# Kernel tuning notes

Measured on AMD Instinct MI355X. Metric: run time of the kernel, lower is better.

The kernel has to match this reference:

```python
import jax, jax.numpy as jnp
import numpy as np

N, D = 8192, 512
HEADS, DIM_HEAD, M, ITERS = 8, 64, 256, 6
WP = 256          # CustomAttention weight_params_dim
E = 262144        # number of adjacency edges
K = 33            # residual depthwise conv kernel


def setup_inputs():
    key = jax.random.key(0)
    ks = jax.random.split(key, 12)
    inner = HEADS * DIM_HEAD
    xav = (6.0 / (D + WP)) ** 0.5
    return {
        "dense": jax.random.normal(ks[0], (N, D), jnp.float32),
        "adj_rows": jax.random.randint(ks[1], (E,), 0, N, dtype=jnp.int32),
        "adj_cols": jax.random.randint(ks[2], (E,), 0, N, dtype=jnp.int32),
        "adj_vals": jnp.ones((E,), jnp.float32),
        "wq": jax.random.uniform(ks[3], (D, WP), jnp.float32, -xav, xav),
        "wk": jax.random.uniform(ks[4], (D, WP), jnp.float32, -xav, xav),
        "w_qkv": jax.random.normal(ks[5], (3 * inner, D), jnp.float32) * D ** -0.5,
        "w_out": jax.random.normal(ks[6], (D, inner), jnp.float32) * inner ** -0.5,
        "b_out": jnp.zeros((D,), jnp.float32),
        "res_kernel": jax.random.normal(ks[7], (HEADS, 1, K, 1), jnp.float32) * 0.05,
        "wv_w": jax.random.normal(ks[8], (D, D), jnp.float32) * D ** -0.5,
        "wv_b": jnp.zeros((D,), jnp.float32),
    }


def _pinv(x, iters):
    # Moore-Penrose iterative pseudo-inverse (lucidrains nystrom-attention)
    ax = jnp.abs(x)
    z = jnp.swapaxes(x, -1, -2) / (ax.sum(-1).max() * ax.sum(-2).max())
    I = jnp.eye(x.shape[-1], dtype=x.dtype)
    for _ in range(iters):
        xz = x @ z
        z = 0.25 * z @ (13.0 * I - xz @ (15.0 * I - xz @ (7.0 * I - xz)))
    return z


def _nystrom(x, w_qkv, w_out, b_out, res_kernel):
    # x: [n, dim]; batch of 1 in original (squeezed here)
    n = x.shape[0]
    pad = (-n) % M
    xp = jnp.pad(x, ((pad, 0), (0, 0)))  # pad at front, as in original
    n_p = n + pad
    qkv = xp @ w_qkv.T  # [n_p, 3*h*d]
    q, k, v = [t.reshape(n_p, HEADS, DIM_HEAD).transpose(1, 0, 2)
               for t in jnp.split(qkv, 3, axis=-1)]  # each [h, n_p, d]
    q = q * DIM_HEAD ** -0.5
    l = n_p // M
    q_l = q.reshape(HEADS, M, l, DIM_HEAD).mean(2)  # [h, m, d] landmark means
    k_l = k.reshape(HEADS, M, l, DIM_HEAD).mean(2)
    a1 = jax.nn.softmax(jnp.einsum('hid,hjd->hij', q, k_l), -1)    # [h, n_p, m]
    a2 = jax.nn.softmax(jnp.einsum('hid,hjd->hij', q_l, k_l), -1)  # [h, m, m]
    a3 = jax.nn.softmax(jnp.einsum('hid,hjd->hij', q_l, k), -1)    # [h, m, n_p]
    out = (a1 @ _pinv(a2, ITERS)) @ (a3 @ v)  # [h, n_p, d]
    # residual depthwise conv over sequence dim, per head (groups=heads)
    res = jax.lax.conv_general_dilated(
        v[None], res_kernel, (1, 1), ((K // 2, K // 2), (0, 0)),
        dimension_numbers=('NCHW', 'OIHW', 'NCHW'), feature_group_count=HEADS)[0]
    out = out + res
    out = out.transpose(1, 0, 2).reshape(n_p, HEADS * DIM_HEAD) @ w_out.T + b_out
    return out[-n:]


def reference(dense, adj_rows, adj_cols, adj_vals, wq, wk, w_qkv, w_out, b_out,
              res_kernel, wv_w, wv_b):
    xg = _nystrom(dense, w_qkv, w_out, b_out, res_kernel)
    enc = xg + dense                              # [N, D]
    q = enc @ wq
    k = enc @ wk
    att = (q @ k.T) * (WP ** -0.5)                # [N, N] scaled logits
    # sparse adjacency mask + row-sum (torch.sparse.sum over dim=1)
    edge_scores = att[adj_rows, adj_cols] * adj_vals
    A_raw = jax.ops.segment_sum(edge_scores, adj_rows, num_segments=dense.shape[0])
    alpha = jax.nn.softmax(A_raw)                 # softmax over all N instances
    value = dense @ wv_w.T + wv_b                 # [N, D]
    xl = alpha[:, None] * value
    wei = jax.nn.sigmoid(-xl)
    sq = wei * wei
    xo = xl * 2.0 * sq + 2.0 * enc * (1.0 - sq)   # gated residual blend
    return xo, A_raw
```

## Files before the change

### kernel.cpp

```cpp
#include <hip/hip_runtime.h>
#include <hip/hip_bf16.h>

#define NSEQ 8192
#define DDIM 512
#define HEADS 8
#define DH 64
#define MLM 256
#define LSUB 32
#define WP 256
#define KCONV 33
#define INNER 512
#define QKV_LD 1536

static const size_t OFF_QKVBF  = 0;
static const size_t OFF_VT     = 6291456;
static const size_t OFF_SC     = 8388608;
static const size_t OFF_A2     = 8388608;
static const size_t OFF_Z0     = 8912896;
static const size_t OFF_Z1     = 9437184;
static const size_t OFF_P      = 9961472;
static const size_t OFF_T1     = 10485760;
static const size_t OFF_T2     = 11010048;
static const size_t OFF_QKE    = 10485760;
static const size_t OFF_ATTNBF = 12582912;
static const size_t OFF_ATTN   = 16777216;
static const size_t OFF_ENC    = 0;
static const size_t OFF_ENCBF  = 4194304;
static const size_t OFF_VAL    = 6291456;
static const size_t OFF_DENSEBF= 20971520;
static const size_t OFF_WQKVBF = 23068672;
static const size_t OFF_WOUTBF = 23461888;
static const size_t OFF_WQKT   = 23592960;
static const size_t OFF_WVBF   = 23724032;
static const size_t OFF_QL     = 23855104;
static const size_t OFF_KL     = 23986176;
static const size_t OFF_QLBF   = 24117248;
static const size_t OFF_KLSBF  = 24182784;
static const size_t OFF_A3V    = 24248320;
static const size_t OFF_BB     = 24379392;
static const size_t OFF_BBT    = 24510464;
static const size_t OFF_SCAL   = 24576000;
static const size_t OFF_ALPHA  = 24576016;
static const size_t OFF_DEN3   = 24584208;

__device__ __forceinline__ float bf2f(unsigned short u) {
    return __uint_as_float(((unsigned int)u) << 16);
}
__device__ __forceinline__ unsigned short f2bf(float x) {
    unsigned int u = __float_as_uint(x);
    u += 0x7FFFu + ((u >> 16) & 1u);
    return (unsigned short)(u >> 16);
}

typedef __attribute__((ext_vector_type(8))) short bf16x8;
typedef __attribute__((ext_vector_type(4))) float f32x4;

__device__ __forceinline__ void gload_lds16(const void* g, void* l) {
    __builtin_amdgcn_global_load_lds(
// ... 19 lines not shown
    const float* __restrict__ in, unsigned short* __restrict__ out, int R, int C)
{
    int idx = blockIdx.x * 256 + threadIdx.x;
    if (idx < R * C) {
        int oc = idx / R;
        int orow = idx % R;
        out[idx] = f2bf(in[(size_t)orow * C + oc]);
    }
}

__global__ __launch_bounds__(256) void gemm_mfma_ntb(
    const unsigned short* __restrict__ A, int lda, size_t sA,
    const unsigned short* __restrict__ B, int ldb, size_t sB,
    float* __restrict__ C, unsigned short* __restrict__ Cbf, int ldc, size_t sC,
    int K, const float* __restrict__ bias, const float* __restrict__ addsrc,
    int expmode)
{
    __shared__ __align__(16) unsigned short As[64 * 64];
    __shared__ __align__(16) unsigned short Bs[128 * 64];
    const int tid = threadIdx.x;
    const int wave = tid >> 6, lane = tid & 63;
    const int l15 = lane & 15, l4 = lane >> 4;
    const int wm = wave >> 1, wn = wave & 1;
    const size_t bm = (size_t)blockIdx.x * 64;
    const size_t bn = (size_t)blockIdx.y * 128;
    const int z = blockIdx.z;
    const unsigned short* Ab = A + (size_t)z * sA;
    const unsigned short* Bb = B + (size_t)z * sB;
    const int swzr = (l15 & 7) << 3;
    f32x4 acc[2][4] = {};
    for (int k0 = 0; k0 < K; k0 += 64) {
        __syncthreads();
#pragma unroll
        for (int c2 = 0; c2 < 2; ++c2) {
            int id = c2 * 256 + tid;
            int row = id >> 3;
            int cg = ((id & 7) ^ (row & 7)) << 3;
            gload_lds16(Ab + (bm + row) * (size_t)lda + k0 + cg, As + id * 8);
        }
#pragma unroll
        for (int c2 = 0; c2 < 4; ++c2) {
            int id = c2 * 256 + tid;
            int row = id >> 3;
            int cg = ((id & 7) ^ (row & 7)) << 3;
            gload_lds16(Bb + (bn + row) * (size_t)ldb + k0 + cg, Bs + id * 8);
        }
        __syncthreads();
#pragma unroll
        for (int c = 0; c < 2; ++c) {
            bf16x8 af[2], bfv[4];
#pragma unroll
            for (int i = 0; i < 2; ++i)
                af[i] = *reinterpret_cast<const bf16x8*>(
                    &As[(wm * 32 + i * 16 + l15) * 64 + ((c * 32 + l4 * 8) ^ swzr)]);
#pragma unroll
            for (int j = 0; j < 4; ++j)
                bfv[j] = *reinterpret_cast<const bf16x8*>(
                    &Bs[(wn * 64 + j * 16 + l15) * 64 + ((c * 32 + l4 * 8) ^ swzr)]);
#pragma unroll
            for (int i = 0; i < 2; ++i)
#pragma unroll
                for (int j = 0; j < 4; ++j)
                    acc[i][j] = __builtin_amdgcn_mfma_f32_16x16x32_bf16(
                        af[i], bfv[j], acc[i][j], 0, 0, 0);
        }
    }
    float* Cz = C ? C + (size_t)z * sC : nullptr;
    unsigned short* Cbz = Cbf ? Cbf + (size_t)z * sC : nullptr;
#pragma unroll
    for (int i = 0; i < 2; ++i)
#pragma unroll
        for (int j = 0; j < 4; ++j)
#pragma unroll
            for (int r = 0; r < 4; ++r) {
                size_t row = bm + wm * 32 + i * 16 + l4 * 4 + r;
                size_t col = bn + wn * 64 + j * 16 + l15;
                float v = acc[i][j][r];
                if (bias)   v += bias[col];
                if (addsrc) v += addsrc[row * (size_t)ldc + col];
                if (expmode) v = __expf(v);
                if (Cz)  Cz[row * (size_t)ldc + col] = v;
                if (Cbz) Cbz[row * (size_t)ldc + col] = f2bf(v);
            }
}

__global__ __launch_bounds__(256) void bmm_split(
    const float* __restrict__ A, const float* __restrict__ B, float* __restrict__ C,
    int K, int N, int ntn, size_t sA, size_t sB, size_t sC, float alpha, float beta)
{
    __shared__ __align__(16) unsigned short Ah[64 * 72], Al[64 * 72];
    __shared__ __align__(16) unsigned short Bh[64 * 72], Bl[64 * 72];
    const int tid = threadIdx.x;
    const int wave = tid >> 6, lane = tid & 63;
    const int l15 = lane & 15, l4 = lane >> 4;
    const int wm = wave >> 1, wn = wave & 1;
    const int b = blockIdx.y;
    const int tm = blockIdx.x / ntn, tn = blockIdx.x % ntn;
    const float* Ab = A + (size_t)b * sA;
    const float* Bb = B + (size_t)b * sB;
    float* Cb = C + (size_t)b * sC;
    const int arow = tid >> 2, akq = (tid & 3) * 16;
    const int kp = tid & 31, nc = tid >> 5;
    f32x4 acc[2][2] = {};
    for (int k0 = 0; k0 < K; k0 += 64) {
        __syncthreads();
#pragma unroll
        for (int s = 0; s < 4; ++s) {
            float4 a = *reinterpret_cast<const float4*>(Ab + (size_t)(tm * 64 + arow) * K + k0 + akq + s * 4);
            unsigned short h0 = f2bf(a.x), h1 = f2bf(a.y), h2 = f2bf(a.z), h3 = f2bf(a.w);
            unsigned short g0 = f2bf(a.x - bf2f(h0)), g1 = f2bf(a.y - bf2f(h1));
            unsigned short g2 = f2bf(a.z - bf2f(h2)), g3 = f2bf(a.w - bf2f(h3));
            uint2 ph, pl;
            ph.x = h0 | ((unsigned int)h1 << 16); ph.y = h2 | ((unsigned int)h3 << 16);
            pl.x = g0 | ((unsigned int)g1 << 16); pl.y = g2 | ((unsigned int)g3 << 16);
            *reinterpret_cast<uint2*>(&Ah[arow * 72 + akq + s * 4]) = ph;
            *reinterpret_cast<uint2*>(&Al[arow * 72 + akq + s * 4]) = pl;
        }
#pragma unroll
        for (int s = 0; s < 2; ++s) {
            int cb = nc * 8 + s * 4;
            float4 b0 = *reinterpret_cast<const float4*>(Bb + (size_t)(k0 + 2 * kp) * N + tn * 64 + cb);
            float4 b1 = *reinterpret_cast<const float4*>(Bb + (size_t)(k0 + 2 * kp + 1) * N + tn * 64 + cb);
            float x0[4] = {b0.x, b0.y, b0.z, b0.w};
            float x1[4] = {b1.x, b1.y, b1.z, b1.w};
#pragma unroll
            for (int c = 0; c < 4; ++c) {
                unsigned short h0 = f2bf(x0[c]), h1 = f2bf(x1[c]);
                unsigned short g0 = f2bf(x0[c] - bf2f(h0)), g1 = f2bf(x1[c] - bf2f(h1));
                *reinterpret_cast<unsigned int*>(&Bh[(cb + c) * 72 + 2 * kp]) =
                    h0 | ((unsigned int)h1 << 16);
                *reinterpret_cast<unsigned int*>(&Bl[(cb + c) * 72 + 2 * kp]) =
                    g0 | ((unsigned int)g1 << 16);
            }
        }
        __syncthreads();
#pragma unroll
        for (int ks = 0; ks < 2; ++ks) {
            bf16x8 ah[2], al[2], bh[2], bl[2];
#pragma unroll
            for (int i = 0; i < 2; ++i) {
                int rr = (wm * 32 + i * 16 + l15) * 72 + ks * 32 + l4 * 8;
                ah[i] = *reinterpret_cast<const bf16x8*>(&Ah[rr]);
                al[i] = *reinterpret_cast<const bf16x8*>(&Al[rr]);
            }
#pragma unroll
            for (int j = 0; j < 2; ++j) {
                int rr = (wn * 32 + j * 16 + l15) * 72 + ks * 32 + l4 * 8;
                bh[j] = *reinterpret_cast<const bf16x8*>(&Bh[rr]);
                bl[j] = *reinterpret_cast<const bf16x8*>(&Bl[rr]);
            }
#pragma unroll
            for (int i = 0; i < 2; ++i)
#pragma unroll
                for (int j = 0; j < 2; ++j) {
                    acc[i][j] = __builtin_amdgcn_mfma_f32_16x16x32_bf16(ah[i], bh[j], acc[i][j], 0, 0, 0);
                    acc[i][j] = __builtin_amdgcn_mfma_f32_16x16x32_bf16(ah[i], bl[j], acc[i][j], 0, 0, 0);
                    acc[i][j] = __builtin_amdgcn_mfma_f32_16x16x32_bf16(al[i], bh[j], acc[i][j], 0, 0, 0);
                }
        }
    }
#pragma unroll
    for (int i = 0; i < 2; ++i)
#pragma unroll
        for (int j = 0; j < 2; ++j)
#pragma unroll
            for (int r = 0; r < 4; ++r) {
                int row = tm * 64 + wm * 32 + i * 16 + l4 * 4 + r;
                int col = tn * 64 + wn * 32 + j * 16 + l15;
                float v = beta * acc[i][j][r];
                if (alpha != 0.f) v += alpha * Ab[(size_t)row * K + col];
                Cb[(size_t)row * N + col] = v;
            }
}

__global__ __launch_bounds__(256) void pv3_mfma(
    const unsigned short* __restrict__ sc, const unsigned short* __restrict__ vT,
    float* __restrict__ part)
{
    __shared__ __align__(16) unsigned short As[64 * 64];
    __shared__ __align__(16) unsigned short Bs[64 * 64];
    const int tid = threadIdx.x;
    const int wave = tid >> 6, lane = tid & 63;
    const int l15 = lane & 15, l4 = lane >> 4;
    const int wm = wave >> 1, wn = wave & 1;
    const int it = blockIdx.x, kc = blockIdx.y, h = blockIdx.z;
    const unsigned short* Ap = sc + (size_t)h * MLM * NSEQ + (size_t)(it * 64) * NSEQ + kc * 512;
// ... 37 lines not shown
    }
    float* Cp = part + ((size_t)(kc * 8 + h) * MLM + it * 64) * DH;
#pragma unroll
    for (int i = 0; i < 2; ++i)
#pragma unroll
        for (int j = 0; j < 2; ++j)
#pragma unroll
            for (int r = 0; r < 4; ++r)
                Cp[(wm * 32 + i * 16 + l4 * 4 + r) * DH + wn * 32 + j * 16 + l15] = acc[i][j][r];
}

__global__ __launch_bounds__(256) void a1_fused(
    const unsigned short* __restrict__ qkvbf,
    const unsigned short* __restrict__ kls,
    const unsigned short* __restrict__ bbT,
    float* __restrict__ attn)
{
    __shared__ __align__(16) unsigned short lds[20480];
    __shared__ float den[2][64];
    const int tid = threadIdx.x;
    const int wave = tid >> 6, lane = tid & 63;
    const int l15 = lane & 15, l4 = lane >> 4;
    const int wm = wave >> 1, wn = wave & 1;
    const int n0 = blockIdx.x * 64;
    const int h = blockIdx.y;
    const int swzr = (l15 & 7) << 3;

#pragma unroll
    for (int c2 = 0; c2 < 2; ++c2) {
        int id = c2 * 256 + tid;
        int row = id >> 3, cg = ((id & 7) ^ (row & 7)) << 3;
        gload_lds16(qkvbf + (size_t)(n0 + row) * QKV_LD + h * DH + cg, lds + id * 8);
    }
#pragma unroll
    for (int c2 = 0; c2 < 8; ++c2) {
        int id = c2 * 256 + tid;
        int row = id >> 3, cg = ((id & 7) ^ (row & 7)) << 3;
        gload_lds16(kls + (size_t)h * (MLM * DH) + row * DH + cg, lds + 4096 + id * 8);
    }
    __syncthreads();
    f32x4 acc[2][8] = {};
#pragma unroll
// ... 49 lines not shown
            int row = wm * 32 + i * 16 + l15;
            af2[i] = *reinterpret_cast<const bf16x8*>(
                &lds[4096 + row * 256 + ((k0 + l4 * 8) ^ ((row & 7) << 3))]);
        }
#pragma unroll
        for (int j = 0; j < 2; ++j) {
            int d = wn * 32 + j * 16 + l15;
            bv2[j] = *reinterpret_cast<const bf16x8*>(&bbh[d * MLM + k0 + l4 * 8]);
        }
#pragma unroll
        for (int i = 0; i < 2; ++i)
#pragma unroll
            for (int j = 0; j < 2; ++j)
                acc2[i][j] = __builtin_amdgcn_mfma_f32_16x16x32_bf16(af2[i], bv2[j], acc2[i][j], 0, 0, 0);
    }
#pragma unroll
    for (int i = 0; i < 2; ++i)
#pragma unroll
        for (int r = 0; r < 4; ++r) {
            int row = wm * 32 + i * 16 + l4 * 4 + r;
            float inv = 1.f / (den[0][row] + den[1][row]);
#pragma unroll
            for (int j = 0; j < 2; ++j)
                attn[(size_t)(n0 + row) * INNER + h * DH + wn * 32 + j * 16 + l15]
                    = acc2[i][j][r] * inv;
        }
}

__global__ __launch_bounds__(64) void landmark2_k(
    const unsigned short* __restrict__ qkvbf, float* __restrict__ q_l, float* __restrict__ k_l,
    unsigned short* __restrict__ ql_bf, unsigned short* __restrict__ kls_bf)
{
    int m = blockIdx.x, h = blockIdx.y, d = threadIdx.x;
    float sq = 0.f, sk = 0.f;
    for (int i = 0; i < LSUB; ++i) {
        size_t n = (size_t)m * LSUB + i;
        sq += bf2f(qkvbf[n * QKV_LD + h * DH + d]);
        sk += bf2f(qkvbf[n * QKV_LD + 512 + h * DH + d]);
    }
    float qv = sq * (0.125f / (float)LSUB);
    float kv = sk * (1.f / (float)LSUB);
// ... 17 lines not shown
        uint4 v = *reinterpret_cast<const uint4*>(
            qkvbf + (size_t)(n0 + row) * QKV_LD + 1024 + h * 64 + ch);
        *reinterpret_cast<uint4*>(&tile[row][ch]) = v;
    }
    __syncthreads();
#pragma unroll
    for (int s = 0; s < 4; ++s) {
        int cid = s * 256 + t;
        int d = cid >> 4, nch = (cid & 15) * 8;
        unsigned short o[8];
#pragma unroll
        for (int i = 0; i < 8; ++i) o[i] = tile[nch + i][d];
        *reinterpret_cast<uint4*>(vT + (size_t)h * DH * NSEQ + (size_t)d * NSEQ + n0 + nch) =
            *reinterpret_cast<uint4*>(o);
    }
}

__global__ __launch_bounds__(256) void bbt_k(
    const float* __restrict__ bb, unsigned short* __restrict__ bbT)
{
    int idx = blockIdx.x * 256 + threadIdx.x;
    int h = idx >> 14, rem = idx & 16383;
    int d = rem >> 8, j = rem & 255;
    bbT[idx] = f2bf(bb[(h << 14) + (j << 6) + d]);
}

__global__ __launch_bounds__(256) void a2_k(
    const float* __restrict__ q_l, const float* __restrict__ k_l, float* __restrict__ a2)
{
    int i = blockIdx.x, h = blockIdx.y, t = threadIdx.x;
    __shared__ float ql[64];
    __shared__ float red[256];
    if (t < 64) ql[t] = q_l[((size_t)h * MLM + i) * DH + t];
    __syncthreads();
    const float* kr = k_l + ((size_t)h * MLM + t) * DH;
    float s = 0.f;
#pragma unroll
    for (int d = 0; d < 64; d += 4) {
        float4 kv = *reinterpret_cast<const float4*>(kr + d);
// ... 14 lines not shown
    int b = blockIdx.x, t = threadIdx.x;
    __shared__ float red[256];
    float sum = 0.f;
    if (b < 8) {
        const float* r = a2 + ((size_t)b * MLM + t) * MLM;
        for (int j = 0; j < MLM; ++j) sum += fabsf(r[j]);
    } else {
        int h = b - 8;
        for (int i = 0; i < MLM; ++i) sum += fabsf(a2[((size_t)h * MLM + i) * MLM + t]);
    }
    red[t] = sum; __syncthreads();
    for (int off = 128; off > 0; off >>= 1) { if (t < off) red[t] = fmaxf(red[t], red[t + off]); __syncthreads(); }
    if (t == 0) atomicMax(scal + (b < 8 ? 0 : 1), __float_as_uint(red[0]));
}

__global__ __launch_bounds__(256) void zinit_k(
    const float* __restrict__ a2, const unsigned int* __restrict__ scal, float* __restrict__ z)
{
    int idx = blockIdx.x * 256 + threadIdx.x;
    float rmax = __uint_as_float(scal[0]);
    float cmax = __uint_as_float(scal[1]);
    float inv = 1.f / (rmax * cmax);
    int h = idx >> 16, rem = idx & 65535, i = rem >> 8, j = rem & 255;
    z[idx] = a2[((size_t)h << 16) + (j << 8) + i] * inv;
}

__global__ __launch_bounds__(256) void den3_k(
    const unsigned short* __restrict__ sc, float* __restrict__ den3)
{
    __shared__ float red[256];
    const int t = threadIdx.x;
    const unsigned short* row = sc + (size_t)blockIdx.x * NSEQ;
    float s = 0.f;
#pragma unroll
    for (int u = 0; u < 4; ++u) {
        uint4 pk = *reinterpret_cast<const uint4*>(row + t * 32 + u * 8);
        unsigned int w[4] = {pk.x, pk.y, pk.z, pk.w};
#pragma unroll
        for (int q = 0; q < 4; ++q) {
            s += bf2f((unsigned short)(w[q] & 0xFFFF));
            s += bf2f((unsigned short)(w[q] >> 16));
        }
    }
    red[t] = s; __syncthreads();
    for (int off = 128; off > 0; off >>= 1) { if (t < off) red[t] += red[t + off]; __syncthreads(); }
    if (t == 0) den3[blockIdx.x] = red[0];
}

__global__ __launch_bounds__(256) void red3_k(
    const float* __restrict__ part, const float* __restrict__ den3,
    float* __restrict__ a3v)
{
    int o = blockIdx.x * 256 + threadIdx.x;
    float s = 0.f;
#pragma unroll
    for (int kc = 0; kc < 16; ++kc) s += part[(size_t)kc * 131072 + o];
    a3v[o] = s / den3[o >> 6];
}

__global__ __launch_bounds__(256) void conv_res2_k(
    const unsigned short* __restrict__ qkvbf, const float* __restrict__ kern,
    float* __restrict__ attn)
{
    const int t = threadIdx.x;
    const int cg = (blockIdx.y * 64 + (t & 63)) * 4;
    const int n0 = blockIdx.x * 32 + (t >> 6) * 8;
    const int h = cg >> 6;
    float kr[KCONV];
#pragma unroll
    for (int i = 0; i < KCONV; ++i) kr[i] = kern[h * KCONV + i];
    float acc[8][4] = {};
#pragma unroll
    for (int r = 0; r < 40; ++r) {
        int nn = n0 + r - 16;
        float v0 = 0.f, v1 = 0.f, v2 = 0.f, v3 = 0.f;
        if (nn >= 0 && nn < NSEQ) {
            ushort4 u = *reinterpret_cast<const ushort4*>(qkvbf + (size_t)nn * QKV_LD + 1024 + cg);
            v0 = bf2f(u.x); v1 = bf2f(u.y); v2 = bf2f(u.z); v3 = bf2f(u.w);
        }
#pragma unroll
        for (int j = 0; j < 8; ++j) {
            int tt = r - j;
            if (tt >= 0 && tt < KCONV) {
                acc[j][0] += kr[tt] * v0; acc[j][1] += kr[tt] * v1;
                acc[j][2] += kr[tt] * v2; acc[j][3] += kr[tt] * v3;
            }
        }
    }
#pragma unroll
    for (int j = 0; j < 8; ++j) {
        float4* p = reinterpret_cast<float4*>(attn + (size_t)(n0 + j) * INNER + cg);
        float4 c = *p;
        c.x += acc[j][0]; c.y += acc[j][1]; c.z += acc[j][2]; c.w += acc[j][3];
        *p = c;
    }
}

__global__ __launch_bounds__(256) void edge2_k(
    const unsigned short* __restrict__ qke,
    const int* __restrict__ rows, const int* __restrict__ cols,
    const float* __restrict__ vals, float* __restrict__ A_raw)
{
    const int e = blockIdx.x * 32 + (threadIdx.x >> 3);
    const int g = threadIdx.x & 7;
    const int r = rows[e], c = cols[e];
    const unsigned short* qr = qke + (size_t)r * 512 + g * 32;
    const unsigned short* kr = qke + (size_t)c * 512 + 256 + g * 32;
    float s = 0.f;
#pragma unroll
    for (int u = 0; u < 4; ++u) {
// ... 17 lines not shown
    __shared__ float red[1024];
    int t = threadIdx.x;
    float m = -1e30f;
    for (int i = t; i < NSEQ; i += 1024) m = fmaxf(m, A_raw[i]);
    red[t] = m; __syncthreads();
    for (int off = 512; off > 0; off >>= 1) { if (t < off) red[t] = fmaxf(red[t], red[t + off]); __syncthreads(); }
    m = red[0]; __syncthreads();
    float s = 0.f;
    for (int i = t; i < NSEQ; i += 1024) s += __expf(A_raw[i] - m);
    red[t] = s; __syncthreads();
    for (int off = 512; off > 0; off >>= 1) { if (t < off) red[t] += red[t + off]; __syncthreads(); }
    float inv = 1.f / red[0];
    for (int i = t; i < NSEQ; i += 1024) alpha[i] = __expf(A_raw[i] - m) * inv;
}

__global__ __launch_bounds__(256) void final_k(
    const float* __restrict__ alpha, const float* __restrict__ value,
    const float* __restrict__ enc, float* __restrict__ xo)
{
    size_t idx = (size_t)blockIdx.x * 256 + threadIdx.x;
    int n = (int)(idx >> 9);
    float xl = alpha[n] * value[idx];
    float w = 1.f / (1.f + __expf(xl));
    float sq = w * w;
    xo[idx] = xl * 2.f * sq + 2.f * enc[idx] * (1.f - sq);
}

extern "C" void kernel_launch(void* const* d_in, const int* in_sizes, int n_in,
                              void* d_out, int out_size, void* d_ws, size_t ws_size,
                              hipStream_t stream)
{
    const float* dense      = (const float*)d_in[0];
    const int*   adj_rows   = (const int*)d_in[1];
    const int*   adj_cols   = (const int*)d_in[2];
    const float* adj_vals   = (const float*)d_in[3];
    const float* wq         = (const float*)d_in[4];
    const float* wk         = (const float*)d_in[5];
    const float* w_qkv      = (const float*)d_in[6];
    const float* w_out      = (const float*)d_in[7];
    const float* b_out      = (const float*)d_in[8];
    const float* res_kernel = (const float*)d_in[9];
    const float* wv_w       = (const float*)d_in[10];
    const float* wv_b       = (const float*)d_in[11];
    const int E = in_sizes[1];

    float* ws  = (float*)d_ws;
    float* out = (float*)d_out;
    float* A_raw = out + (size_t)NSEQ * DDIM;

    unsigned short* qkv_bf   = (unsigned short*)(ws + OFF_QKVBF);
    unsigned short* vT       = (unsigned short*)(ws + OFF_VT);
    unsigned short* sc       = (unsigned short*)(ws + OFF_SC);
    unsigned short* qke_bf   = (unsigned short*)(ws + OFF_QKE);
    unsigned short* attn_bf  = (unsigned short*)(ws + OFF_ATTNBF);
    unsigned short* dense_bf = (unsigned short*)(ws + OFF_DENSEBF);
    unsigned short* wqkv_bf  = (unsigned short*)(ws + OFF_WQKVBF);
    unsigned short* wout_bf  = (unsigned short*)(ws + OFF_WOUTBF);
    unsigned short* wqkT_bf  = (unsigned short*)(ws + OFF_WQKT);
    unsigned short* wv_bf    = (unsigned short*)(ws + OFF_WVBF);
    unsigned short* ql_bf    = (unsigned short*)(ws + OFF_QLBF);
    unsigned short* kls_bf   = (unsigned short*)(ws + OFF_KLSBF);
    unsigned short* bbT_bf   = (unsigned short*)(ws + OFF_BBT);
    unsigned short* enc_bf   = (unsigned short*)(ws + OFF_ENCBF);

    hipMemsetAsync(A_raw, 0, NSEQ * sizeof(float), stream);
    hipMemsetAsync(ws + OFF_SCAL, 0, 2 * sizeof(unsigned int), stream);

    cvt_bf16_k<<<(NSEQ * DDIM) / 2048, 256, 0, stream>>>(dense, dense_bf);
    cvt_bf16_k<<<(1536 * DDIM) / 2048, 256, 0, stream>>>(w_qkv, wqkv_bf);

    gemm_mfma_ntb<<<dim3(NSEQ / 64, 1536 / 128, 1), 256, 0, stream>>>(
        dense_bf, DDIM, 0, wqkv_bf, DDIM, 0, nullptr, qkv_bf, QKV_LD, 0,
        DDIM, nullptr, nullptr, 0);

    landmark2_k<<<dim3(MLM, HEADS), 64, 0, stream>>>(
        qkv_bf, ws + OFF_QL, ws + OFF_KL, ql_bf, kls_bf);
    vt_k<<<dim3(NSEQ / 128, HEADS), 256, 0, stream>>>(qkv_bf, vT);

    gemm_mfma_ntb<<<dim3(MLM / 64, NSEQ / 128, HEADS), 256, 0, stream>>>(
        ql_bf, DH, (size_t)MLM * DH, qkv_bf + 512, QKV_LD, DH,
        nullptr, sc, NSEQ, (size_t)MLM * NSEQ, DH, nullptr, nullptr, 1);
    den3_k<<<HEADS * MLM, 256, 0, stream>>>(sc, ws + OFF_DEN3);
    pv3_mfma<<<dim3(4, 16, HEADS), 256, 0, stream>>>(sc, vT, ws + OFF_ATTN);
    red3_k<<<512, 256, 0, stream>>>(ws + OFF_ATTN, ws + OFF_DEN3, ws + OFF_A3V);

    a2_k<<<dim3(MLM, HEADS), 256, 0, stream>>>(ws + OFF_QL, ws + OFF_KL, ws + OFF_A2);
    absmax_k<<<16, 256, 0, stream>>>(ws + OFF_A2, (unsigned int*)(ws + OFF_SCAL));
    zinit_k<<<(HEADS * MLM * MLM) / 256, 256, 0, stream>>>(
        ws + OFF_A2, (const unsigned int*)(ws + OFF_SCAL), ws + OFF_Z0);

    for (int it = 0; it < 6; ++it) {
        float* zin  = ws + ((it & 1) ? OFF_Z1 : OFF_Z0);
        float* zout = ws + ((it & 1) ? OFF_Z0 : OFF_Z1);
        bmm_split<<<dim3(16, HEADS), 256, 0, stream>>>(ws + OFF_A2, zin, ws + OFF_P,
            256, 256, 4, 65536, 65536, 65536, 0.f, 1.f);
        bmm_split<<<dim3(16, HEADS), 256, 0, stream>>>(ws + OFF_P, ws + OFF_P, ws + OFF_T1,
            256, 256, 4, 65536, 65536, 65536, 7.f, -1.f);
        bmm_split<<<dim3(16, HEADS), 256, 0, stream>>>(ws + OFF_P, ws + OFF_T1, ws + OFF_T2,
            256, 256, 4, 65536, 65536, 65536, 15.f, -1.f);
        bmm_split<<<dim3(16, HEADS), 256, 0, stream>>>(zin, ws + OFF_T2, zout,
            256, 256, 4, 65536, 65536, 65536, 3.25f, -0.25f);
    }
    bmm_split<<<dim3(4, HEADS), 256, 0, stream>>>(ws + OFF_Z0, ws + OFF_A3V, ws + OFF_BB,
        256, 64, 1, 65536, 16384, 16384, 0.f, 1.f);
    bbt_k<<<512, 256, 0, stream>>>(ws + OFF_BB, bbT_bf);

    a1_fused<<<dim3(NSEQ / 64, HEADS), 256, 0, stream>>>(
        qkv_bf, kls_bf, bbT_bf, ws + OFF_ATTN);
    conv_res2_k<<<dim3(NSEQ / 32, 2), 256, 0, stream>>>(qkv_bf, res_kernel, ws + OFF_ATTN);

    cvt_bf16_k<<<(NSEQ * INNER) / 2048, 256, 0, stream>>>(ws + OFF_ATTN, attn_bf);
    cvt_bf16_k<<<(DDIM * INNER) / 2048, 256, 0, stream>>>(w_out, wout_bf);
    tcvt_bf16_k<<<(WP * DDIM + 255) / 256, 256, 0, stream>>>(wq, wqkT_bf, DDIM, WP);
    tcvt_bf16_k<<<(WP * DDIM + 255) / 256, 256, 0, stream>>>(wk, wqkT_bf + 256 * 512, DDIM, WP);
    cvt_bf16_k<<<(DDIM * DDIM) / 2048, 256, 0, stream>>>(wv_w, wv_bf);

    gemm_mfma_ntb<<<dim3(NSEQ / 64, DDIM / 128, 1), 256, 0, stream>>>(
        attn_bf, INNER, 0, wout_bf, INNER, 0, ws + OFF_ENC, enc_bf, DDIM, 0,
        INNER, b_out, dense, 0);

    gemm_mfma_ntb<<<dim3(NSEQ / 64, 512 / 128, 1), 256, 0, stream>>>(
        enc_bf, DDIM, 0, wqkT_bf, DDIM, 0, nullptr, qke_bf, 512, 0,
        DDIM, nullptr, nullptr, 0);

    edge2_k<<<E / 32, 256, 0, stream>>>(qke_bf, adj_rows, adj_cols, adj_vals, A_raw);
    alpha_k<<<1, 1024, 0, stream>>>(A_raw, ws + OFF_ALPHA);

    cvt_bf16_k<<<(NSEQ * DDIM) / 2048, 256, 0, stream>>>(dense, dense_bf);
    gemm_mfma_ntb<<<dim3(NSEQ / 64, DDIM / 128, 1), 256, 0, stream>>>(
        dense_bf, DDIM, 0, wv_bf, DDIM, 0, ws + OFF_VAL, nullptr, DDIM, 0,
        DDIM, wv_b, nullptr, 0);

    final_k<<<(NSEQ * DDIM) / 256, 256, 0, stream>>>(
        ws + OFF_ALPHA, ws + OFF_VAL, ws + OFF_ENC, out);
}
```

Measured before the change: 586.1 us.

## Fuse conv residual, final gate and bf16 split storage; enlarge GEMM tiles

Several changes land together. The Newton-Schulz pinv matmuls now keep their operands pre-split into bf16 hi/lo pairs in row and transposed layouts, so each GEMM loads them directly into LDS instead of converting fp32 per tile. The depthwise conv residual and the bf16 conversion are fused into the a1 attention kernel. The final sigmoid gate blend is fused into the value GEMM epilogue, and the redundant dense re-conversion is dropped. The main GEMM tile grows from 64x128 to 128x128, which roughly halves block count and raises register and LDS use per block.

```diff
diff --git a/kernel.cpp b/kernel.cpp
--- a/kernel.cpp
+++ b/kernel.cpp
@@ -15,18 +15,24 @@
 static const size_t OFF_QKVBF  = 0;
 static const size_t OFF_VT     = 6291456;
 static const size_t OFF_SC     = 8388608;
-static const size_t OFF_A2     = 8388608;
-static const size_t OFF_Z0     = 8912896;
-static const size_t OFF_Z1     = 9437184;
-static const size_t OFF_P      = 9961472;
-static const size_t OFF_T1     = 10485760;
-static const size_t OFF_T2     = 11010048;
-static const size_t OFF_QKE    = 10485760;
-static const size_t OFF_ATTNBF = 12582912;
-static const size_t OFF_ATTN   = 16777216;
+#define PS (8388608)
+static const size_t A2R_H = PS + 0;
+static const size_t A2R_L = PS + 262144;
+static const size_t Z0R_H = PS + 524288,  Z0R_L = PS + 786432;
+static const size_t Z0T_H = PS + 1048576, Z0T_L = PS + 1310720;
+static const size_t Z1R_H = PS + 1572864, Z1R_L = PS + 1835008;
+static const size_t Z1T_H = PS + 2097152, Z1T_L = PS + 2359296;
+static const size_t PR_H  = PS + 2621440, PR_L  = PS + 2883584;
+static const size_t PT_H  = PS + 3145728, PT_L  = PS + 3407872;
+static const size_t T1T_H = PS + 3670016, T1T_L = PS + 3932160;
+static const size_t T2T_H = PS + 4194304, T2T_L = PS + 4456448;
+static const size_t A3VT_H= PS + 4718592, A3VT_L= PS + 4784128;
+static const size_t A2F32 = PS + 4849664;
+static const size_t OFF_ATTNBF = 16777216;
+static const size_t OFF_PART   = 18874368;
 static const size_t OFF_ENC    = 0;
 static const size_t OFF_ENCBF  = 4194304;
-static const size_t OFF_VAL    = 6291456;
+static const size_t OFF_QKE    = 6291456;
 static const size_t OFF_DENSEBF= 20971520;
 static const size_t OFF_WQKVBF = 23068672;
 static const size_t OFF_WOUTBF = 23461888;
@@ -36,12 +42,10 @@
 static const size_t OFF_KL     = 23986176;
 static const size_t OFF_QLBF   = 24117248;
 static const size_t OFF_KLSBF  = 24182784;
-static const size_t OFF_A3V    = 24248320;
-static const size_t OFF_BB     = 24379392;
-static const size_t OFF_BBT    = 24510464;
-static const size_t OFF_SCAL   = 24576000;
-static const size_t OFF_ALPHA  = 24576016;
-static const size_t OFF_DEN3   = 24584208;
+static const size_t OFF_BBT    = 24248320;
+static const size_t OFF_SCAL   = 24313856;
+static const size_t OFF_ALPHA  = 24313872;
+static const size_t OFF_DEN3   = 24322064;
 
 __device__ __forceinline__ float bf2f(unsigned short u) {
     return __uint_as_float(((unsigned int)u) << 16);
@@ -91,25 +95,25 @@
     const unsigned short* __restrict__ B, int ldb, size_t sB,
     float* __restrict__ C, unsigned short* __restrict__ Cbf, int ldc, size_t sC,
     int K, const float* __restrict__ bias, const float* __restrict__ addsrc,
-    int expmode)
-{
-    __shared__ __align__(16) unsigned short As[64 * 64];
+    const float* __restrict__ alphav, int epi)
+{
+    __shared__ __align__(16) unsigned short As[128 * 64];
     __shared__ __align__(16) unsigned short Bs[128 * 64];
     const int tid = threadIdx.x;
     const int wave = tid >> 6, lane = tid & 63;
     const int l15 = lane & 15, l4 = lane >> 4;
     const int wm = wave >> 1, wn = wave & 1;
-    const size_t bm = (size_t)blockIdx.x * 64;
+    const size_t bm = (size_t)blockIdx.x * 128;
     const size_t bn = (size_t)blockIdx.y * 128;
     const int z = blockIdx.z;
     const unsigned short* Ab = A + (size_t)z * sA;
     const unsigned short* Bb = B + (size_t)z * sB;
     const int swzr = (l15 & 7) << 3;
-    f32x4 acc[2][4] = {};
+    f32x4 acc[4][4] = {};
     for (int k0 = 0; k0 < K; k0 += 64) {
         __syncthreads();
 #pragma unroll
-        for (int c2 = 0; c2 < 2; ++c2) {
+        for (int c2 = 0; c2 < 4; ++c2) {
             int id = c2 * 256 + tid;
             int row = id >> 3;
             int cg = ((id & 7) ^ (row & 7)) << 3;
@@ -125,17 +129,17 @@
         __syncthreads();
 #pragma unroll
         for (int c = 0; c < 2; ++c) {
-            bf16x8 af[2], bfv[4];
-#pragma unroll
-            for (int i = 0; i < 2; ++i)
+            bf16x8 af[4], bfv[4];
+#pragma unroll
+            for (int i = 0; i < 4; ++i)
                 af[i] = *reinterpret_cast<const bf16x8*>(
-                    &As[(wm * 32 + i * 16 + l15) * 64 + ((c * 32 + l4 * 8) ^ swzr)]);
+                    &As[(wm * 64 + i * 16 + l15) * 64 + ((c * 32 + l4 * 8) ^ swzr)]);
 #pragma unroll
             for (int j = 0; j < 4; ++j)
                 bfv[j] = *reinterpret_cast<const bf16x8*>(
                     &Bs[(wn * 64 + j * 16 + l15) * 64 + ((c * 32 + l4 * 8) ^ swzr)]);
 #pragma unroll
-            for (int i = 0; i < 2; ++i)
+            for (int i = 0; i < 4; ++i)
 #pragma unroll
                 for (int j = 0; j < 4; ++j)
                     acc[i][j] = __builtin_amdgcn_mfma_f32_16x16x32_bf16(
@@ -145,86 +149,80 @@
     float* Cz = C ? C + (size_t)z * sC : nullptr;
     unsigned short* Cbz = Cbf ? Cbf + (size_t)z * sC : nullptr;
 #pragma unroll
-    for (int i = 0; i < 2; ++i)
+    for (int i = 0; i < 4; ++i)
 #pragma unroll
         for (int j = 0; j < 4; ++j)
 #pragma unroll
             for (int r = 0; r < 4; ++r) {
-                size_t row = bm + wm * 32 + i * 16 + l4 * 4 + r;
+                size_t row = bm + wm * 64 + i * 16 + l4 * 4 + r;
                 size_t col = bn + wn * 64 + j * 16 + l15;
                 float v = acc[i][j][r];
-                if (bias)   v += bias[col];
-                if (addsrc) v += addsrc[row * (size_t)ldc + col];
-                if (expmode) v = __expf(v);
-                if (Cz)  Cz[row * (size_t)ldc + col] = v;
-                if (Cbz) Cbz[row * (size_t)ldc + col] = f2bf(v);
+                if (bias) v += bias[col];
+                if (epi == 2) {
+                    float xl = alphav[row] * v;
+                    float w = 1.f / (1.f + __expf(xl));
+                    float sq = w * w;
+                    v = xl * 2.f * sq + 2.f * addsrc[row * (size_t)ldc + col] * (1.f - sq);
+                    Cz[row * (size_t)ldc + col] = v;
+                } else {
+                    if (addsrc) v += addsrc[row * (size_t)ldc + col];
+                    if (epi == 1) v = __expf(v);
+                    if (Cz)  Cz[row * (size_t)ldc + col] = v;
+                    if (Cbz) Cbz[row * (size_t)ldc + col] = f2bf(v);
+                }
             }
 }
 
-__global__ __launch_bounds__(256) void bmm_split(
-    const float* __restrict__ A, const float* __restrict__ B, float* __restrict__ C,
-    int K, int N, int ntn, size_t sA, size_t sB, size_t sC, float alpha, float beta)
-{
-    __shared__ __align__(16) unsigned short Ah[64 * 72], Al[64 * 72];
-    __shared__ __align__(16) unsigned short Bh[64 * 72], Bl[64 * 72];
+__global__ __launch_bounds__(256) void bmm_ps(
+    const unsigned short* __restrict__ Ah, const unsigned short* __restrict__ Al,
+    const unsigned short* __restrict__ Bh, const unsigned short* __restrict__ Bl,
+    unsigned short* __restrict__ Crh, unsigned short* __restrict__ Crl,
+    unsigned short* __restrict__ Cth, unsigned short* __restrict__ Ctl,
+    int M, int N, int K, int ntn, float alpha, float beta)
+{
+    __shared__ __align__(16) unsigned short LAh[64 * 64], LAl[64 * 64];
+    __shared__ __align__(16) unsigned short LBh[64 * 64], LBl[64 * 64];
     const int tid = threadIdx.x;
     const int wave = tid >> 6, lane = tid & 63;
     const int l15 = lane & 15, l4 = lane >> 4;
     const int wm = wave >> 1, wn = wave & 1;
     const int b = blockIdx.y;
     const int tm = blockIdx.x / ntn, tn = blockIdx.x % ntn;
-    const float* Ab = A + (size_t)b * sA;
-    const float* Bb = B + (size_t)b * sB;
-    float* Cb = C + (size_t)b * sC;
-    const int arow = tid >> 2, akq = (tid & 3) * 16;
-    const int kp = tid & 31, nc = tid >> 5;
+    const unsigned short* Ahb = Ah + (size_t)b * M * K;
+    const unsigned short* Alb = Al + (size_t)b * M * K;
+    const unsigned short* Bhb = Bh + (size_t)b * N * K;
+    const unsigned short* Blb = Bl + (size_t)b * N * K;
+    const int swzr = (l15 & 7) << 3;
     f32x4 acc[2][2] = {};
     for (int k0 = 0; k0 < K; k0 += 64) {
         __syncthreads();
 #pragma unroll
-        for (int s = 0; s < 4; ++s) {
-            float4 a = *reinterpret_cast<const float4*>(Ab + (size_t)(tm * 64 + arow) * K + k0 + akq + s * 4);
-            unsigned short h0 = f2bf(a.x), h1 = f2bf(a.y), h2 = f2bf(a.z), h3 = f2bf(a.w);
-            unsigned short g0 = f2bf(a.x - bf2f(h0)), g1 = f2bf(a.y - bf2f(h1));
-            unsigned short g2 = f2bf(a.z - bf2f(h2)), g3 = f2bf(a.w - bf2f(h3));
-            uint2 ph, pl;
-            ph.x = h0 | ((unsigned int)h1 << 16); ph.y = h2 | ((unsigned int)h3 << 16);
-            pl.x = g0 | ((unsigned int)g1 << 16); pl.y = g2 | ((unsigned int)g3 << 16);
-            *reinterpret_cast<uint2*>(&Ah[arow * 72 + akq + s * 4]) = ph;
-            *reinterpret_cast<uint2*>(&Al[arow * 72 + akq + s * 4]) = pl;
-        }
-#pragma unroll
-        for (int s = 0; s < 2; ++s) {
-            int cb = nc * 8 + s * 4;
-            float4 b0 = *reinterpret_cast<const float4*>(Bb + (size_t)(k0 + 2 * kp) * N + tn * 64 + cb);
-            float4 b1 = *reinterpret_cast<const float4*>(Bb + (size_t)(k0 + 2 * kp + 1) * N + tn * 64 + cb);
-            float x0[4] = {b0.x, b0.y, b0.z, b0.w};
-            float x1[4] = {b1.x, b1.y, b1.z, b1.w};
-#pragma unroll
-            for (int c = 0; c < 4; ++c) {
-                unsigned short h0 = f2bf(x0[c]), h1 = f2bf(x1[c]);
-                unsigned short g0 = f2bf(x0[c] - bf2f(h0)), g1 = f2bf(x1[c] - bf2f(h1));
-                *reinterpret_cast<unsigned int*>(&Bh[(cb + c) * 72 + 2 * kp]) =
-                    h0 | ((unsigned int)h1 << 16);
-                *reinterpret_cast<unsigned int*>(&Bl[(cb + c) * 72 + 2 * kp]) =
-                    g0 | ((unsigned int)g1 << 16);
+        for (int c2 = 0; c2 < 2; ++c2) {
+            int id = c2 * 256 + tid;
+            int row = id >> 3;
+            int cg = ((id & 7) ^ (row & 7)) << 3;
+            size_t ao = (size_t)(tm * 64 + row) * K + k0 + cg;
+            size_t bo = (size_t)(tn * 64 + row) * K + k0 + cg;
+            gload_lds16(Ahb + ao, LAh + id * 8);
+            gload_lds16(Alb + ao, LAl + id * 8);
+            gload_lds16(Bhb + bo, LBh + id * 8);
+            gload_lds16(Blb + bo, LBl + id * 8);
+        }
+        __syncthreads();
+#pragma unroll
+        for (int c = 0; c < 2; ++c) {
+            bf16x8 ah[2], al[2], bh[2], bl[2];
+#pragma unroll
+            for (int i = 0; i < 2; ++i) {
+                int rr = (wm * 32 + i * 16 + l15) * 64 + ((c * 32 + l4 * 8) ^ swzr);
+                ah[i] = *reinterpret_cast<const bf16x8*>(&LAh[rr]);
+                al[i] = *reinterpret_cast<const bf16x8*>(&LAl[rr]);
             }
-        }
-        __syncthreads();
-#pragma unroll
-        for (int ks = 0; ks < 2; ++ks) {
-            bf16x8 ah[2], al[2], bh[2], bl[2];
-#pragma unroll
-            for (int i = 0; i < 2; ++i) {
-                int rr = (wm * 32 + i * 16 + l15) * 72 + ks * 32 + l4 * 8;
-                ah[i] = *reinterpret_cast<const bf16x8*>(&Ah[rr]);
-                al[i] = *reinterpret_cast<const bf16x8*>(&Al[rr]);
-            }
 #pragma unroll
             for (int j = 0; j < 2; ++j) {
-                int rr = (wn * 32 + j * 16 + l15) * 72 + ks * 32 + l4 * 8;
-                bh[j] = *reinterpret_cast<const bf16x8*>(&Bh[rr]);
-                bl[j] = *reinterpret_cast<const bf16x8*>(&Bl[rr]);
+                int rr = (wn * 32 + j * 16 + l15) * 64 + ((c * 32 + l4 * 8) ^ swzr);
+                bh[j] = *reinterpret_cast<const bf16x8*>(&LBh[rr]);
+                bl[j] = *reinterpret_cast<const bf16x8*>(&LBl[rr]);
             }
 #pragma unroll
             for (int i = 0; i < 2; ++i)
@@ -236,6 +234,10 @@
                 }
         }
     }
+    unsigned short* Crhb = Crh ? Crh + (size_t)b * M * N : nullptr;
+    unsigned short* Crlb = Crl ? Crl + (size_t)b * M * N : nullptr;
+    unsigned short* Cthb = Cth ? Cth + (size_t)b * M * N : nullptr;
+    unsigned short* Ctlb = Ctl ? Ctl + (size_t)b * M * N : nullptr;
 #pragma unroll
     for (int i = 0; i < 2; ++i)
 #pragma unroll
@@ -245,8 +247,20 @@
                 int row = tm * 64 + wm * 32 + i * 16 + l4 * 4 + r;
                 int col = tn * 64 + wn * 32 + j * 16 + l15;
                 float v = beta * acc[i][j][r];
-                if (alpha != 0.f) v += alpha * Ab[(size_t)row * K + col];
-                Cb[(size_t)row * N + col] = v;
+                if (alpha != 0.f) {
+                    size_t ai = (size_t)row * K + col;
+                    v += alpha * (bf2f(Ahb[ai]) + bf2f(Alb[ai]));
+                }
+                unsigned short hi = f2bf(v);
+                unsigned short lo = f2bf(v - bf2f(hi));
+                if (Crhb) {
+                    Crhb[(size_t)row * N + col] = hi;
+                    if (Crlb) Crlb[(size_t)row * N + col] = lo;
+                }
+                if (Cthb) {
+                    Cthb[(size_t)col * M + row] = hi;
+                    Ctlb[(size_t)col * M + row] = lo;
+                }
             }
 }
 
@@ -314,10 +328,12 @@
     const unsigned short* __restrict__ qkvbf,
     const unsigned short* __restrict__ kls,
     const unsigned short* __restrict__ bbT,
-    float* __restrict__ attn)
+    const float* __restrict__ kern,
+    unsigned short* __restrict__ attnbf)
 {
     __shared__ __align__(16) unsigned short lds[20480];
     __shared__ float den[2][64];
+    __shared__ float kc_s[KCONV];
     const int tid = threadIdx.x;
     const int wave = tid >> 6, lane = tid & 63;
     const int l15 = lane & 15, l4 = lane >> 4;
@@ -326,6 +342,7 @@
     const int h = blockIdx.y;
     const int swzr = (l15 & 7) << 3;
 
+    if (tid < KCONV) kc_s[tid] = kern[h * KCONV + tid];
 #pragma unroll
     for (int c2 = 0; c2 < 2; ++c2) {
         int id = c2 * 256 + tid;
@@ -405,6 +422,9 @@
             for (int j = 0; j < 2; ++j)
                 acc2[i][j] = __builtin_amdgcn_mfma_f32_16x16x32_bf16(af2[i], bv2[j], acc2[i][j], 0, 0, 0);
     }
+    __syncthreads();
+    float* att = reinterpret_cast<float*>(&lds[4096]);
+    unsigned short* vbuf = &lds[12288];
 #pragma unroll
     for (int i = 0; i < 2; ++i)
 #pragma unroll
@@ -413,9 +433,31 @@
             float inv = 1.f / (den[0][row] + den[1][row]);
 #pragma unroll
             for (int j = 0; j < 2; ++j)
-                attn[(size_t)(n0 + row) * INNER + h * DH + wn * 32 + j * 16 + l15]
-                    = acc2[i][j][r] * inv;
-        }
+                att[row * 64 + wn * 32 + j * 16 + l15] = acc2[i][j][r] * inv;
+        }
+#pragma unroll
+    for (int s = 0; s < 6; ++s) {
+        int id = s * 256 + tid;
+        int r = id >> 4, c4 = (id & 15) * 4;
+        int n = n0 - 16 + r;
+        ushort4 u = {0, 0, 0, 0};
+        if (n >= 0 && n < NSEQ)
+            u = *reinterpret_cast<const ushort4*>(qkvbf + (size_t)n * QKV_LD + 1024 + h * 64 + c4);
+        *reinterpret_cast<ushort4*>(vbuf + r * 64 + c4) = u;
+    }
+    __syncthreads();
+    const int col = tid & 63, rowg = tid >> 6;
+    float vwin[48];
+#pragma unroll
+    for (int t = 0; t < 48; ++t) vwin[t] = bf2f(vbuf[(rowg * 16 + t) * 64 + col]);
+#pragma unroll
+    for (int rr = 0; rr < 16; ++rr) {
+        float cv = 0.f;
+#pragma unroll
+        for (int t = 0; t < KCONV; ++t) cv += kc_s[t] * vwin[rr + t];
+        int row = rowg * 16 + rr;
+        attnbf[(size_t)(n0 + row) * INNER + h * DH + col] = f2bf(att[row * 64 + col] + cv);
+    }
 }
 
 __global__ __launch_bounds__(64) void landmark2_k(
@@ -463,15 +505,6 @@
         *reinterpret_cast<uint4*>(vT + (size_t)h * DH * NSEQ + (size_t)d * NSEQ + n0 + nch) =
             *reinterpret_cast<uint4*>(o);
     }
-}
-
-__global__ __launch_bounds__(256) void bbt_k(
-    const float* __restrict__ bb, unsigned short* __restrict__ bbT)
-{
-    int idx = blockIdx.x * 256 + threadIdx.x;
-    int h = idx >> 14, rem = idx & 16383;
-    int d = rem >> 8, j = rem & 255;
-    bbT[idx] = f2bf(bb[(h << 14) + (j << 6) + d]);
 }
 
 __global__ __launch_bounds__(256) void a2_k(
@@ -516,15 +549,24 @@
     if (t == 0) atomicMax(scal + (b < 8 ? 0 : 1), __float_as_uint(red[0]));
 }
 
-__global__ __launch_bounds__(256) void zinit_k(
-    const float* __restrict__ a2, const unsigned int* __restrict__ scal, float* __restrict__ z)
+__global__ __launch_bounds__(256) void zinit2_k(
+    const float* __restrict__ a2, const unsigned int* __restrict__ scal,
+    unsigned short* __restrict__ a2h, unsigned short* __restrict__ a2l,
+    unsigned short* __restrict__ zrh, unsigned short* __restrict__ zrl,
+    unsigned short* __restrict__ zth, unsigned short* __restrict__ ztl)
 {
     int idx = blockIdx.x * 256 + threadIdx.x;
-    float rmax = __uint_as_float(scal[0]);
-    float cmax = __uint_as_float(scal[1]);
-    float inv = 1.f / (rmax * cmax);
+    float inv = 1.f / (__uint_as_float(scal[0]) * __uint_as_float(scal[1]));
     int h = idx >> 16, rem = idx & 65535, i = rem >> 8, j = rem & 255;
-    z[idx] = a2[((size_t)h << 16) + (j << 8) + i] * inv;
+    float aij = a2[idx];
+    unsigned short h1 = f2bf(aij);
+    a2h[idx] = h1; a2l[idx] = f2bf(aij - bf2f(h1));
+    float zt = aij * inv;
+    unsigned short h2 = f2bf(zt);
+    zth[idx] = h2; ztl[idx] = f2bf(zt - bf2f(h2));
+    float zr = a2[((size_t)h << 16) + (j << 8) + i] * inv;
+    unsigned short h3 = f2bf(zr);
+    zrh[idx] = h3; zrl[idx] = f2bf(zr - bf2f(h3));
 }
 
 __global__ __launch_bounds__(256) void den3_k(
@@ -551,51 +593,17 @@
 
 __global__ __launch_bounds__(256) void red3_k(
     const float* __restrict__ part, const float* __restrict__ den3,
-    float* __restrict__ a3v)
+    unsigned short* __restrict__ a3vth, unsigned short* __restrict__ a3vtl)
 {
     int o = blockIdx.x * 256 + threadIdx.x;
     float s = 0.f;
 #pragma unroll
     for (int kc = 0; kc < 16; ++kc) s += part[(size_t)kc * 131072 + o];
-    a3v[o] = s / den3[o >> 6];
-}
-
-__global__ __launch_bounds__(256) void conv_res2_k(
-    const unsigned short* __restrict__ qkvbf, const float* __restrict__ kern,
-    float* __restrict__ attn)
-{
-    const int t = threadIdx.x;
-    const int cg = (blockIdx.y * 64 + (t & 63)) * 4;
-    const int n0 = blockIdx.x * 32 + (t >> 6) * 8;
-    const int h = cg >> 6;
-    float kr[KCONV];
-#pragma unroll
-    for (int i = 0; i < KCONV; ++i) kr[i] = kern[h * KCONV + i];
-    float acc[8][4] = {};
-#pragma unroll
-    for (int r = 0; r < 40; ++r) {
-        int nn = n0 + r - 16;
-        float v0 = 0.f, v1 = 0.f, v2 = 0.f, v3 = 0.f;
-        if (nn >= 0 && nn < NSEQ) {
-            ushort4 u = *reinterpret_cast<const ushort4*>(qkvbf + (size_t)nn * QKV_LD + 1024 + cg);
-            v0 = bf2f(u.x); v1 = bf2f(u.y); v2 = bf2f(u.z); v3 = bf2f(u.w);
-        }
-#pragma unroll
-        for (int j = 0; j < 8; ++j) {
-            int tt = r - j;
-            if (tt >= 0 && tt < KCONV) {
-                acc[j][0] += kr[tt] * v0; acc[j][1] += kr[tt] * v1;
-                acc[j][2] += kr[tt] * v2; acc[j][3] += kr[tt] * v3;
-            }
-        }
-    }
-#pragma unroll
-    for (int j = 0; j < 8; ++j) {
-        float4* p = reinterpret_cast<float4*>(attn + (size_t)(n0 + j) * INNER + cg);
-        float4 c = *p;
-        c.x += acc[j][0]; c.y += acc[j][1]; c.z += acc[j][2]; c.w += acc[j][3];
-        *p = c;
-    }
+    s /= den3[o >> 6];
+    int h = o >> 14, i = (o >> 6) & 255, d = o & 63;
+    int to = (h << 14) + (d << 8) + i;
+    unsigned short hi = f2bf(s);
+    a3vth[to] = hi; a3vtl[to] = f2bf(s - bf2f(hi));
 }
 
 __global__ __launch_bounds__(256) void edge2_k(
@@ -643,18 +651,6 @@
     for (int i = t; i < NSEQ; i += 1024) alpha[i] = __expf(A_raw[i] - m) * inv;
 }
 
-__global__ __launch_bounds__(256) void final_k(
-    const float* __restrict__ alpha, const float* __restrict__ value,
-    const float* __restrict__ enc, float* __restrict__ xo)
-{
-    size_t idx = (size_t)blockIdx.x * 256 + threadIdx.x;
-    int n = (int)(idx >> 9);
-    float xl = alpha[n] * value[idx];
-    float w = 1.f / (1.f + __expf(xl));
-    float sq = w * w;
-    xo[idx] = xl * 2.f * sq + 2.f * enc[idx] * (1.f - sq);
-}
-
 extern "C" void kernel_launch(void* const* d_in, const int* in_sizes, int n_in,
                               void* d_out, int out_size, void* d_ws, size_t ws_size,
                               hipStream_t stream)
@@ -680,8 +676,8 @@
     unsigned short* qkv_bf   = (unsigned short*)(ws + OFF_QKVBF);
     unsigned short* vT       = (unsigned short*)(ws + OFF_VT);
     unsigned short* sc       = (unsigned short*)(ws + OFF_SC);
+    unsigned short* attn_bf  = (unsigned short*)(ws + OFF_ATTNBF);
     unsigned short* qke_bf   = (unsigned short*)(ws + OFF_QKE);
-    unsigned short* attn_bf  = (unsigned short*)(ws + OFF_ATTNBF);
     unsigned short* dense_bf = (unsigned short*)(ws + OFF_DENSEBF);
     unsigned short* wqkv_bf  = (unsigned short*)(ws + OFF_WQKVBF);
     unsigned short* wout_bf  = (unsigned short*)(ws + OFF_WOUTBF);
@@ -692,74 +688,78 @@
     unsigned short* bbT_bf   = (unsigned short*)(ws + OFF_BBT);
     unsigned short* enc_bf   = (unsigned short*)(ws + OFF_ENCBF);
 
+#define U16(off) ((unsigned short*)(ws + (off)))
+
     hipMemsetAsync(A_raw, 0, NSEQ * sizeof(float), stream);
     hipMemsetAsync(ws + OFF_SCAL, 0, 2 * sizeof(unsigned int), stream);
 
     cvt_bf16_k<<<(NSEQ * DDIM) / 2048, 256, 0, stream>>>(dense, dense_bf);
     cvt_bf16_k<<<(1536 * DDIM) / 2048, 256, 0, stream>>>(w_qkv, wqkv_bf);
 
-    gemm_mfma_ntb<<<dim3(NSEQ / 64, 1536 / 128, 1), 256, 0, stream>>>(
+    gemm_mfma_ntb<<<dim3(NSEQ / 128, 1536 / 128, 1), 256, 0, stream>>>(
         dense_bf, DDIM, 0, wqkv_bf, DDIM, 0, nullptr, qkv_bf, QKV_LD, 0,
-        DDIM, nullptr, nullptr, 0);
+        DDIM, nullptr, nullptr, nullptr, 0);
 
     landmark2_k<<<dim3(MLM, HEADS), 64, 0, stream>>>(
         qkv_bf, ws + OFF_QL, ws + OFF_KL, ql_bf, kls_bf);
     vt_k<<<dim3(NSEQ / 128, HEADS), 256, 0, stream>>>(qkv_bf, vT);
 
-    gemm_mfma_ntb<<<dim3(MLM / 64, NSEQ / 128, HEADS), 256, 0, stream>>>(
+    gemm_mfma_ntb<<<dim3(MLM / 128, NSEQ / 128, HEADS), 256, 0, stream>>>(
         ql_bf, DH, (size_t)MLM * DH, qkv_bf + 512, QKV_LD, DH,
-        nullptr, sc, NSEQ, (size_t)MLM * NSEQ, DH, nullptr, nullptr, 1);
+        nullptr, sc, NSEQ, (size_t)MLM * NSEQ, DH, nullptr, nullptr, nullptr, 1);
     den3_k<<<HEADS * MLM, 256, 0, stream>>>(sc, ws + OFF_DEN3);
-    pv3_mfma<<<dim3(4, 16, HEADS), 256, 0, stream>>>(sc, vT, ws + OFF_ATTN);
-    red3_k<<<512, 256, 0, stream>>>(ws + OFF_ATTN, ws + OFF_DEN3, ws + OFF_A3V);
-
-    a2_k<<<dim3(MLM, HEADS), 256, 0, stream>>>(ws + OFF_QL, ws + OFF_KL, ws + OFF_A2);
-    absmax_k<<<16, 256, 0, stream>>>(ws + OFF_A2, (unsigned int*)(ws + OFF_SCAL));
-    zinit_k<<<(HEADS * MLM * MLM) / 256, 256, 0, stream>>>(
-        ws + OFF_A2, (const unsigned int*)(ws + OFF_SCAL), ws + OFF_Z0);
+    pv3_mfma<<<dim3(4, 16, HEADS), 256, 0, stream>>>(sc, vT, ws + OFF_PART);
+    red3_k<<<512, 256, 0, stream>>>(ws + OFF_PART, ws + OFF_DEN3,
+                                    U16(A3VT_H), U16(A3VT_L));
+
+    a2_k<<<dim3(MLM, HEADS), 256, 0, stream>>>(ws + OFF_QL, ws + OFF_KL, ws + A2F32);
+    absmax_k<<<16, 256, 0, stream>>>(ws + A2F32, (unsigned int*)(ws + OFF_SCAL));
+    zinit2_k<<<(HEADS * MLM * MLM) / 256, 256, 0, stream>>>(
+        ws + A2F32, (const unsigned int*)(ws + OFF_SCAL),
+        U16(A2R_H), U16(A2R_L), U16(Z0R_H), U16(Z0R_L), U16(Z0T_H), U16(Z0T_L));
 
     for (int it = 0; it < 6; ++it) {
-        float* zin  = ws + ((it & 1) ? OFF_Z1 : OFF_Z0);
-        float* zout = ws + ((it & 1) ? OFF_Z0 : OFF_Z1);
-        bmm_split<<<dim3(16, HEADS), 256, 0, stream>>>(ws + OFF_A2, zin, ws + OFF_P,
-            256, 256, 4, 65536, 65536, 65536, 0.f, 1.f);
-        bmm_split<<<dim3(16, HEADS), 256, 0, stream>>>(ws + OFF_P, ws + OFF_P, ws + OFF_T1,
-            256, 256, 4, 65536, 65536, 65536, 7.f, -1.f);
-        bmm_split<<<dim3(16, HEADS), 256, 0, stream>>>(ws + OFF_P, ws + OFF_T1, ws + OFF_T2,
-            256, 256, 4, 65536, 65536, 65536, 15.f, -1.f);
-        bmm_split<<<dim3(16, HEADS), 256, 0, stream>>>(zin, ws + OFF_T2, zout,
-            256, 256, 4, 65536, 65536, 65536, 3.25f, -0.25f);
-    }
-    bmm_split<<<dim3(4, HEADS), 256, 0, stream>>>(ws + OFF_Z0, ws + OFF_A3V, ws + OFF_BB,
-        256, 64, 1, 65536, 16384, 16384, 0.f, 1.f);
-    bbt_k<<<512, 256, 0, stream>>>(ws + OFF_BB, bbT_bf);
+        size_t zr_h = (it & 1) ? Z1R_H : Z0R_H, zr_l = (it & 1) ? Z1R_L : Z0R_L;
+        size_t zt_h = (it & 1) ? Z1T_H : Z0T_H, zt_l = (it & 1) ? Z1T_L : Z0T_L;
+        size_t or_h = (it & 1) ? Z0R_H : Z1R_H, or_l = (it & 1) ? Z0R_L : Z1R_L;
+        size_t ot_h = (it & 1) ? Z0T_H : Z1T_H, ot_l = (it & 1) ? Z0T_L : Z1T_L;
+        bmm_ps<<<dim3(16, HEADS), 256, 0, stream>>>(
+            U16(A2R_H), U16(A2R_L), U16(zt_h), U16(zt_l),
+            U16(PR_H), U16(PR_L), U16(PT_H), U16(PT_L), 256, 256, 256, 4, 0.f, 1.f);
+        bmm_ps<<<dim3(16, HEADS), 256, 0, stream>>>(
+            U16(PR_H), U16(PR_L), U16(PT_H), U16(PT_L),
+            nullptr, nullptr, U16(T1T_H), U16(T1T_L), 256, 256, 256, 4, 7.f, -1.f);
+        bmm_ps<<<dim3(16, HEADS), 256, 0, stream>>>(
+            U16(PR_H), U16(PR_L), U16(T1T_H), U16(T1T_L),
+            nullptr, nullptr, U16(T2T_H), U16(T2T_L), 256, 256, 256, 4, 15.f, -1.f);
+        bmm_ps<<<dim3(16, HEADS), 256, 0, stream>>>(
+            U16(zr_h), U16(zr_l), U16(T2T_H), U16(T2T_L),
+            U16(or_h), U16(or_l), U16(ot_h), U16(ot_l), 256, 256, 256, 4, 3.25f, -0.25f);
+    }
+    bmm_ps<<<dim3(4, HEADS), 256, 0, stream>>>(
+        U16(A3VT_H), U16(A3VT_L), U16(Z0R_H), U16(Z0R_L),
+        bbT_bf, nullptr, nullptr, nullptr, 64, 256, 256, 4, 0.f, 1.f);
 
     a1_fused<<<dim3(NSEQ / 64, HEADS), 256, 0, stream>>>(
-        qkv_bf, kls_bf, bbT_bf, ws + OFF_ATTN);
-    conv_res2_k<<<dim3(NSEQ / 32, 2), 256, 0, stream>>>(qkv_bf, res_kernel, ws + OFF_ATTN);
-
-    cvt_bf16_k<<<(NSEQ * INNER) / 2048, 256, 0, stream>>>(ws + OFF_ATTN, attn_bf);
+        qkv_bf, kls_bf, bbT_bf, res_kernel, attn_bf);
+
     cvt_bf16_k<<<(DDIM * INNER) / 2048, 256, 0, stream>>>(w_out, wout_bf);
     tcvt_bf16_k<<<(WP * DDIM + 255) / 256, 256, 0, stream>>>(wq, wqkT_bf, DDIM, WP);
     tcvt_bf16_k<<<(WP * DDIM + 255) / 256, 256, 0, stream>>>(wk, wqkT_bf + 256 * 512, DDIM, WP);
     cvt_bf16_k<<<(DDIM * DDIM) / 2048, 256, 0, stream>>>(wv_w, wv_bf);
 
-    gemm_mfma_ntb<<<dim3(NSEQ / 64, DDIM / 128, 1), 256, 0, stream>>>(
+    gemm_mfma_ntb<<<dim3(NSEQ / 128, DDIM / 128, 1), 256, 0, stream>>>(
         attn_bf, INNER, 0, wout_bf, INNER, 0, ws + OFF_ENC, enc_bf, DDIM, 0,
-        INNER, b_out, dense, 0);
-
-    gemm_mfma_ntb<<<dim3(NSEQ / 64, 512 / 128, 1), 256, 0, stream>>>(
+        INNER, b_out, dense, nullptr, 0);
+
+    gemm_mfma_ntb<<<dim3(NSEQ / 128, 512 / 128, 1), 256, 0, stream>>>(
         enc_bf, DDIM, 0, wqkT_bf, DDIM, 0, nullptr, qke_bf, 512, 0,
-        DDIM, nullptr, nullptr, 0);
+        DDIM, nullptr, nullptr, nullptr, 0);
 
     edge2_k<<<E / 32, 256, 0, stream>>>(qke_bf, adj_rows, adj_cols, adj_vals, A_raw);
     alpha_k<<<1, 1024, 0, stream>>>(A_raw, ws + OFF_ALPHA);
 
-    cvt_bf16_k<<<(NSEQ * DDIM) / 2048, 256, 0, stream>>>(dense, dense_bf);
-    gemm_mfma_ntb<<<dim3(NSEQ / 64, DDIM / 128, 1), 256, 0, stream>>>(
-        dense_bf, DDIM, 0, wv_bf, DDIM, 0, ws + OFF_VAL, nullptr, DDIM, 0,
-        DDIM, wv_b, nullptr, 0);
-
-    final_k<<<(NSEQ * DDIM) / 256, 256, 0, stream>>>(
-        ws + OFF_ALPHA, ws + OFF_VAL, ws + OFF_ENC, out);
-}
+    gemm_mfma_ntb<<<dim3(NSEQ / 128, DDIM / 128, 1), 256, 0, stream>>>(
+        dense_bf, DDIM, 0, wv_bf, DDIM, 0, out, nullptr, DDIM, 0,
+        DDIM, wv_b, ws + OFF_ENC, ws + OFF_ALPHA, 2);
+}
```

Result: slower. 653.7 us (+11.5%).
